# Performance work log

Hardware: AMD Instinct MI355X
Metric: run time of the kernel (lower is better)

## Reference

```python
import jax, jax.numpy as jnp
import numpy as np

B, T, D, H = 256, 512, 64, 128


def setup_inputs() -> dict:
    key = jax.random.key(0)
    ks = jax.random.split(key, 24)
    inp = {
        'values': jax.random.normal(ks[0], (B, T, D), jnp.float32),
        'masks': jax.random.randint(ks[1], (B, T, D), 0, 2).astype(jnp.float32),
        'deltas': jax.random.uniform(ks[2], (B, T, D), jnp.float32),
        'empirical_mean': jax.random.normal(ks[3], (D,), jnp.float32),
        'X_filledLOCF': jax.random.normal(ks[4], (B, T, D), jnp.float32),
        # parameters (xavier-ish scale for matrices, uniform for vectors)
        'w_gamma_x': jax.random.uniform(ks[5], (D,), jnp.float32),
        'w_gamma_h': jax.random.normal(ks[6], (D, H), jnp.float32) * (2.0 / (D + H)) ** 0.5,
        'w_rx': jax.random.normal(ks[7], (D, H), jnp.float32) * (2.0 / (D + H)) ** 0.5,
        'w_rh': jax.random.normal(ks[8], (H, H), jnp.float32) * (1.0 / H) ** 0.5,
        'w_rm': jax.random.normal(ks[9], (D, H), jnp.float32) * (2.0 / (D + H)) ** 0.5,
        'w_zx': jax.random.normal(ks[10], (D, H), jnp.float32) * (2.0 / (D + H)) ** 0.5,
        'w_zh': jax.random.normal(ks[11], (H, H), jnp.float32) * (1.0 / H) ** 0.5,
        'w_zm': jax.random.normal(ks[12], (D, H), jnp.float32) * (2.0 / (D + H)) ** 0.5,
        'w_hx': jax.random.normal(ks[13], (D, H), jnp.float32) * (2.0 / (D + H)) ** 0.5,
        'w_hh': jax.random.normal(ks[14], (H, H), jnp.float32) * (1.0 / H) ** 0.5,
        'w_hm': jax.random.normal(ks[15], (D, H), jnp.float32) * (2.0 / (D + H)) ** 0.5,
        'b_gamma_x': jax.random.uniform(ks[16], (D,), jnp.float32),
        'b_gamma_h': jax.random.uniform(ks[17], (H,), jnp.float32),
        'b_r': jax.random.uniform(ks[18], (H,), jnp.float32),
        'b_z': jax.random.uniform(ks[19], (H,), jnp.float32),
        'b_h': jax.random.uniform(ks[20], (H,), jnp.float32),
    }
    return inp


def reference(values, masks, deltas, empirical_mean, X_filledLOCF,
              w_gamma_x, w_gamma_h, w_rx, w_rh, w_rm, w_zx, w_zh, w_zm,
              w_hx, w_hh, w_hm, b_gamma_x, b_gamma_h, b_r, b_z, b_h):
    b, t, d = values.shape
    h0 = jnp.zeros((b, w_gamma_h.shape[1]), values.dtype)

    def step(h, xs):
        x, m, dlt, xl = xs  # each [B, D]
        gamma_x = jnp.exp(-jax.nn.relu(w_gamma_x * dlt + b_gamma_x))      # [B, D]
        gamma_h = jnp.exp(-jax.nn.relu(dlt @ w_gamma_h + b_gamma_h))      # [B, H]
        x = m * x + (1 - m) * (gamma_x * xl + (1 - gamma_x) * empirical_mean)
        h = gamma_h * h
        z = jax.nn.sigmoid(x @ w_zx + h @ w_zh + m @ w_zm + b_z)
        r = jax.nn.sigmoid(x @ w_rx + h @ w_rh + m @ w_rm + b_r)
        h_tilde = jnp.tanh(x @ w_hx + (r * h) @ w_hh + m @ w_hm + b_h)
        h = (1 - z) * h + z * h_tilde
        return h, h

    # scan over time axis: [T, B, D]
    xs = (jnp.swapaxes(values, 0, 1), jnp.swapaxes(masks, 0, 1),
          jnp.swapaxes(deltas, 0, 1), jnp.swapaxes(X_filledLOCF, 0, 1))
    h_last, hs = jax.lax.scan(step, h0, xs)
    hidden_tensor = jnp.swapaxes(hs, 0, 1)  # [B, T, H]
    return hidden_tensor, h_last
```

## Files before the change

### kernel.cpp

```cpp
#include <hip/hip_runtime.h>
#include <hip/hip_fp16.h>

#define B_ 256
#define T_ 512
#define D_ 64
#define H_ 128
#define BB 16

typedef float f32x4 __attribute__((ext_vector_type(4)));
typedef short s16x4 __attribute__((ext_vector_type(4)));
typedef short s16x8 __attribute__((ext_vector_type(8)));
typedef __bf16 bf16x8 __attribute__((ext_vector_type(8)));
typedef _Float16 h16x4 __attribute__((ext_vector_type(4)));
typedef _Float16 f16x8v __attribute__((ext_vector_type(8)));

__device__ unsigned short g_W16[7 * 8 * 2 * 512];
__device__ float g_bias[512];

__device__ inline float toF(__half x) { return __half2float(x); }

__device__ inline float fsig(float x) {
  return __builtin_amdgcn_rcpf(1.f + __expf(-x));
}
__device__ inline float ftanh(float x) {
  return 1.f - 2.f * __builtin_amdgcn_rcpf(1.f + __expf(2.f * x));
}
__device__ inline short f2bf(float f) {
  unsigned u = __builtin_bit_cast(unsigned, f);
  u += 0x7fff + ((u >> 16) & 1);
  return (short)(u >> 16);
}
__device__ __forceinline__ f32x4 MF(s16x8 a, s16x8 b, f32x4 c) {
  return __builtin_amdgcn_mfma_f32_16x16x32_bf16(
      __builtin_bit_cast(bf16x8, a), __builtin_bit_cast(bf16x8, b), c, 0, 0, 0);
}
__device__ __forceinline__ f32x4 MFH(f16x8v a, s16x8 b, f32x4 c) {
  return __builtin_amdgcn_mfma_f32_16x16x32_f16(
      a, __builtin_bit_cast(f16x8v, b), c, 0, 0, 0);
}

#define BAR()                                              \
  do {                                                     \
    asm volatile("s_waitcnt lgkmcnt(0)" ::: "memory");     \
    __builtin_amdgcn_s_barrier();                          \
  } while (0)

__global__ __launch_bounds__(64) void wprep(
    const float* __restrict__ wgh, const float* __restrict__ wzx,
    const float* __restrict__ wzm, const float* __restrict__ wrx,
    const float* __restrict__ wrm, const float* __restrict__ whx,
    const float* __restrict__ whm, const float* __restrict__ bgh,
    const float* __restrict__ bz, const float* __restrict__ br,
    const float* __restrict__ bh) {
  const int g = blockIdx.x, l = threadIdx.x;
  if (g < 112) {
    const float* mats[7] = {wgh, wzx, wzm, wrx, wrm, whx, whm};
    const int mat = g >> 4, sub = g & 15, ct = sub >> 1, tau = sub & 1;
    const float* W = mats[mat];
    const int base = ((mat * 8 + ct) * 2 + tau) * 512 + l * 8;
#pragma unroll
    for (int j = 0; j < 8; ++j) {
      const int k = 8 * (l >> 4) + j + 32 * tau;
      const int col = ct * 16 + (l & 15);
      g_W16[base + j] =
          __builtin_bit_cast(unsigned short, __float2half(W[k * 128 + col]));
    }
  } else {
    const int c = (g - 112) * 64 + l;
    float v = (c < 128)   ? bgh[c]
              : (c < 256) ? bz[c - 128]
              : (c < 384) ? br[c - 256]
                          : bh[c - 384];
    g_bias[c] = v;
  }
}

__global__ __launch_bounds__(256) void grud_pre_mfma(
    const float* __restrict__ values, const float* __restrict__ masks,
    const float* __restrict__ deltas, const float* __restrict__ emean,
    const float* __restrict__ locf, const float* __restrict__ w_gamma_x,
    const float* __restrict__ b_gamma_x, __half* __restrict__ A) {
  __shared__ __align__(16) char plds[65536];
  float* c_wg = (float*)(plds + 24576);
  float* c_bg = (float*)(plds + 24832);
  float* c_mn = (float*)(plds + 25088);

  const int tid = threadIdx.x;
  const int rowbase = blockIdx.x * 64;

  if (tid < 64) c_wg[tid] = w_gamma_x[tid];
  else if (tid < 128) c_bg[tid - 64] = b_gamma_x[tid - 64];
  else if (tid < 192) c_mn[tid - 128] = emean[tid - 128];
  __syncthreads();

  {
    const int r = tid >> 2;
    const int sp = tid & 3;
    const int swz = (r & 7) << 4;
#pragma unroll
    for (int ss = 0; ss < 2; ++ss) {
      const int s = sp + 4 * ss;
      const int k0 = 8 * s;
      const size_t gb = (size_t)(rowbase + r) * 64 + k0;
      const float4* vp = (const float4*)(values + gb);
      const float4* mp = (const float4*)(masks + gb);
      const float4* dp = (const float4*)(deltas + gb);
      const float4* lp = (const float4*)(locf + gb);
      float4 v0 = vp[0], v1 = vp[1], m0 = mp[0], m1 = mp[1];
      float4 d0 = dp[0], d1 = dp[1], l0 = lp[0], l1 = lp[1];
      float vv[8] = {v0.x, v0.y, v0.z, v0.w, v1.x, v1.y, v1.z, v1.w};
      float mm[8] = {m0.x, m0.y, m0.z, m0.w, m1.x, m1.y, m1.z, m1.w};
      float dd[8] = {d0.x, d0.y, d0.z, d0.w, d1.x, d1.y, d1.z, d1.w};
      float ll[8] = {l0.x, l0.y, l0.z, l0.w, l1.x, l1.y, l1.z, l1.w};
      s16x8 xe_, mv_, dl_;
#pragma unroll
      for (int j = 0; j < 8; ++j) {
        const int d_ = k0 + j;
        float gx = __expf(-fmaxf(c_wg[d_] * dd[j] + c_bg[d_], 0.f));
        float xo = mm[j] * vv[j] +
                   (1.f - mm[j]) * (gx * ll[j] + (1.f - gx) * c_mn[d_]);
        xe_[j] = __builtin_bit_cast(short, __float2half(xo));
        mv_[j] = __builtin_bit_cast(short, __float2half(mm[j]));
        dl_[j] = __builtin_bit_cast(short, __float2half(dd[j]));
      }
      const int ta = r * 128 + ((s * 16) ^ swz);
      *(s16x8*)(plds + ta) = xe_;
      *(s16x8*)(plds + 8192 + ta) = mv_;
      *(s16x8*)(plds + 16384 + ta) = dl_;
    }
  }
  __syncthreads();

  const int l = tid & 63;
  const int rt = tid >> 6;
  f16x8v xe0, xe1, mm0, mm1, dl0, dl1;
  {
    const int r = rt * 16 + (l & 15);
    const int swz = (r & 7) << 4;
    const int s0 = ((l >> 4) * 16) ^ swz;
    const int s1 = (((l >> 4) + 4) * 16) ^ swz;
    xe0 = *(const f16x8v*)(plds + r * 128 + s0);
    xe1 = *(const f16x8v*)(plds + r * 128 + s1);
    mm0 = *(const f16x8v*)(plds + 8192 + r * 128 + s0);
    mm1 = *(const f16x8v*)(plds + 8192 + r * 128 + s1);
    dl0 = *(const f16x8v*)(plds + 16384 + r * 128 + s0);
    dl1 = *(const f16x8v*)(plds + 16384 + r * 128 + s1);
  }
  __syncthreads();

  const s16x8* Wb = (const s16x8*)g_W16;
  const int cc = l & 15;
#pragma unroll 4
  for (int ct = 0; ct < 32; ++ct) {
    const int g = ct >> 3, ctl = ct & 7;
    f32x4 acc = {0.f, 0.f, 0.f, 0.f};
    if (g == 0) {
      s16x8 B0 = Wb[(ctl * 2 + 0) * 64 + l];
      s16x8 B1 = Wb[(ctl * 2 + 1) * 64 + l];
      acc = MFH(dl0, B0, acc);
      acc = MFH(dl1, B1, acc);
    } else {
      const int mx = 2 * g - 1, mmat = 2 * g;
      s16x8 Bx0 = Wb[((mx * 8 + ctl) * 2 + 0) * 64 + l];
      s16x8 Bx1 = Wb[((mx * 8 + ctl) * 2 + 1) * 64 + l];
      s16x8 Bm0 = Wb[((mmat * 8 + ctl) * 2 + 0) * 64 + l];
      s16x8 Bm1 = Wb[((mmat * 8 + ctl) * 2 + 1) * 64 + l];
      acc = MFH(xe0, Bx0, acc);
      acc = MFH(xe1, Bx1, acc);
      acc = MFH(mm0, Bm0, acc);
      acc = MFH(mm1, Bm1, acc);
    }
    const int c = ct * 16 + cc;
    const float bv = g_bias[c];
#pragma unroll
    for (int j = 0; j < 4; ++j) {
      const int row = rt * 16 + (l >> 4) * 4 + j;
      float v = acc[j] + bv;
      if (ct < 8) v = __expf(-fmaxf(v, 0.f));
      *(unsigned short*)(plds + row * 1024 + ((c * 2) ^ ((row & 7) << 4))) =
          __builtin_bit_cast(unsigned short, __float2half(v));
    }
  }
  __syncthreads();

  {
    const int r = tid >> 2, qq = tid & 3;
    const int swz = (r & 7) << 4;
#pragma unroll
    for (int i = 0; i < 16; ++i) {
      s16x8 v = *(const s16x8*)(plds + r * 1024 + ((qq * 256 + i * 16) ^ swz));
      *(s16x8*)((unsigned short*)A + (size_t)(rowbase + r) * 512 + qq * 128 +
                i * 8) = v;
    }
  }
}

#define STEP(T0, CUR, NXT)                                                  \
  do {                                                                      \
    const int t_ = (T0);                                                    \
    h16x4 tAz = CUR[1], tAr = CUR[2], tAh = CUR[3];                         \
    {                                                                       \
      const int t4 = (t_ + 4 < T_) ? t_ + 4 : T_ - 1;                       \
      const size_t r = ((size_t)bg * T_ + t4) * 128 + ci;                   \
      CUR[0] = Arows[r];       CUR[1] = Arows[r + 32];                      \
      CUR[2] = Arows[r + 64];  CUR[3] = Arows[r + 96];                      \
    }                                                                       \
    f32x4 Dz0 = {0,0,0,0}, Dz1 = {0,0,0,0};                                 \
    f32x4 Dr0 = {0,0,0,0}, Dr1 = {0,0,0,0};                                 \
    {                                                                       \
      s16x8 bh0 = *(const s16x8*)(h_bf + off_rd[0]);                        \
      s16x8 bh1 = *(const s16x8*)(h_bf + off_rd[1]);                        \
      s16x8 bh2 = *(const s16x8*)(h_bf + off_rd[2]);                        \
      s16x8 bh3 = *(const s16x8*)(h_bf + off_rd[3]);                        \
      Dz0 = MF(wzf[0], bh0, Dz0); Dr0 = MF(wrf[0], bh0, Dr0);               \
      Dz1 = MF(wzf[2], bh2, Dz1); Dr1 = MF(wrf[2], bh2, Dr1);               \
      Dz0 = MF(wzf[1], bh1, Dz0); Dr0 = MF(wrf[1], bh1, Dr0);               \
      Dz1 = MF(wzf[3], bh3, Dz1); Dr1 = MF(wrf[3], bh3, Dr1);               \
    }                                                                       \
    f32x4 zz;                                                               \
    s16x4 rhv;                                                              \
    _Pragma("unroll")                                                       \
    for (int j = 0; j < 4; ++j) {                                           \
      zz[j] = fsig((float)tAz[j] + (Dz0[j] + Dz1[j]));                      \
      float rr = fsig((float)tAr[j] + (Dr0[j] + Dr1[j]));                   \
      rhv[j] = f2bf(rr * hsc[j]);                                           \
    }                                                                       \
    *(s16x4*)(rh_bf + off_wr) = rhv;                                        \
    BAR();                                                                  \
    f32x4 Dh0 = {0,0,0,0}, Dh1 = {0,0,0,0};                                 \
    {                                                                       \
      s16x8 p0 = *(const s16x8*)(rh_bf + off_rd[0]);                        \
      s16x8 p1 = *(const s16x8*)(rh_bf + off_rd[1]);                        \
      s16x8 p2 = *(const s16x8*)(rh_bf + off_rd[2]);                        \
      s16x8 p3 = *(const s16x8*)(rh_bf + off_rd[3]);                        \
      Dh0 = MF(whf[0], p0, Dh0); Dh1 = MF(whf[2], p2, Dh1);                 \
      Dh0 = MF(whf[1], p1, Dh0); Dh1 = MF(whf[3], p3, Dh1);                 \
    }                                                                       \
    f32x4 hnv;                                                              \
    s16x4 hbv;                                                              \
    _Pragma("unroll")                                                       \
    for (int j = 0; j < 4; ++j) {                                           \
      float ht = ftanh((float)tAh[j] + (Dh0[j] + Dh1[j]));                  \
      float hn = (1.f - zz[j]) * hsc[j] + zz[j] * ht;                       \
      hnv[j] = hn;                                                          \
      float hg = hn * (float)NXT[0][j];                                     \
      hsc[j] = hg;                                                          \
      hbv[j] = f2bf(hg);                                                    \
    }                                                                       \
    *(f32x4*)(hid + ((size_t)bg * T_ + t_) * H_ + cb) = hnv;                \
    if (t_ == T_ - 1) *(f32x4*)(hlast + (size_t)bg * H_ + cb) = hnv;        \
    *(s16x4*)(h_bf + off_wr) = hbv;                                         \
    BAR();                                                                  \
  } while (0)

__global__ __launch_bounds__(512, 1) void grud_rec_mfma(
    const __half* __restrict__ A, const float* __restrict__ w_zh,
    const float* __restrict__ w_rh, const float* __restrict__ w_hh,
    float* __restrict__ hid, float* __restrict__ hlast) {
  const int tid = threadIdx.x;
  const int w = tid >> 6;
  const int lane = tid & 63;
  const int b = lane & 15;
  const int q = lane >> 4;
  const int cb = w * 16 + q * 4;
  const int bg = blockIdx.x * BB + b;

  __shared__ __align__(16) char lds[8192];
  char* h_bf = lds;
  char* rh_bf = lds + 4096;

  s16x8 wzf[4], wrf[4], whf[4];
#pragma unroll
  for (int tau = 0; tau < 4; ++tau) {
    s16x8 az, ar, ah;
#pragma unroll
    for (int j = 0; j < 8; ++j) {
      const int k = q * 8 + j + 32 * tau;
      az[j] = f2bf(w_zh[k * H_ + w * 16 + b]);
      ar[j] = f2bf(w_rh[k * H_ + w * 16 + b]);
      ah[j] = f2bf(w_hh[k * H_ + w * 16 + b]);
    }
    wzf[tau] = az; wrf[tau] = ar; whf[tau] = ah;
  }

  for (int i = tid; i < 8192 / 16; i += 512)
    ((f32x4*)lds)[i] = f32x4{0.f, 0.f, 0.f, 0.f};

  int off_rd[4];
#pragma unroll
  for (int tau = 0; tau < 4; ++tau) off_rd[tau] = tau * 1024 + lane * 16;
  const int off_wr =
      (w >> 1) * 1024 + (b + 16 * ((2 * w + (q >> 1)) & 3)) * 16 + 8 * (q & 1);

  const h16x4* Arows = (const h16x4*)A;
  const int ci = cb >> 2;

  h16x4 b0[4], b1[4], b2[4], b3[4];
  {
    const size_t r0 = ((size_t)bg * T_ + 0) * 128 + ci;
    b0[0] = Arows[r0]; b0[1] = Arows[r0 + 32];
    b0[2] = Arows[r0 + 64]; b0[3] = Arows[r0 + 96];
    const size_t r1 = ((size_t)bg * T_ + 1) * 128 + ci;
    b1[0] = Arows[r1]; b1[1] = Arows[r1 + 32];
    b1[2] = Arows[r1 + 64]; b1[3] = Arows[r1 + 96];
    const size_t r2 = ((size_t)bg * T_ + 2) * 128 + ci;
    b2[0] = Arows[r2]; b2[1] = Arows[r2 + 32];
    b2[2] = Arows[r2 + 64]; b2[3] = Arows[r2 + 96];
    const size_t r3 = ((size_t)bg * T_ + 3) * 128 + ci;
    b3[0] = Arows[r3]; b3[1] = Arows[r3 + 32];
    b3[2] = Arows[r3 + 64]; b3[3] = Arows[r3 + 96];
  }
  f32x4 hsc = {0.f, 0.f, 0.f, 0.f};
  __syncthreads();

  for (int tp = 0; tp < T_; tp += 4) {
    STEP(tp + 0, b0, b1);
    STEP(tp + 1, b1, b2);
    STEP(tp + 2, b2, b3);
    STEP(tp + 3, b3, b0);
  }
}

extern "C" void kernel_launch(void* const* d_in, const int* in_sizes, int n_in,
                              void* d_out, int out_size, void* d_ws, size_t ws_size,
                              hipStream_t stream) {
  const float* values = (const float*)d_in[0];
  const float* masks = (const float*)d_in[1];
  const float* deltas = (const float*)d_in[2];
  const float* emean = (const float*)d_in[3];
  const float* locf = (const float*)d_in[4];
  const float* w_gamma_x = (const float*)d_in[5];
  const float* w_gamma_h = (const float*)d_in[6];
  const float* w_rx = (const float*)d_in[7];
  const float* w_rh = (const float*)d_in[8];
  const float* w_rm = (const float*)d_in[9];
  const float* w_zx = (const float*)d_in[10];
  const float* w_zh = (const float*)d_in[11];
  const float* w_zm = (const float*)d_in[12];
  const float* w_hx = (const float*)d_in[13];
  const float* w_hh = (const float*)d_in[14];
  const float* w_hm = (const float*)d_in[15];
  const float* b_gamma_x = (const float*)d_in[16];
  const float* b_gamma_h = (const float*)d_in[17];
  const float* b_r = (const float*)d_in[18];
  const float* b_z = (const float*)d_in[19];
  const float* b_h = (const float*)d_in[20];

  float* hid = (float*)d_out;
  float* hlast = hid + (size_t)B_ * T_ * H_;
  __half* A = (__half*)d_ws;

  wprep<<<dim3(120), dim3(64), 0, stream>>>(
      w_gamma_h, w_zx, w_zm, w_rx, w_rm, w_hx, w_hm, b_gamma_h, b_z, b_r, b_h);
  grud_pre_mfma<<<dim3(B_ * T_ / 64), dim3(256), 0, stream>>>(
      values, masks, deltas, emean, locf, w_gamma_x, b_gamma_x, A);
  grud_rec_mfma<<<dim3(B_ / BB), dim3(512), 0, stream>>>(A, w_zh, w_rh, w_hh,
                                                         hid, hlast);
}
```

Baseline: 755.3 us.

## Halve recurrent block to 4 waves with two column tiles each; transpose pre-kernel MFMA output

After: 730.8 us. -3.3%, faster.

```diff
diff --git a/kernel.cpp b/kernel.cpp
--- a/kernel.cpp
+++ b/kernel.cpp
@@ -17,8 +17,6 @@
 __device__ unsigned short g_W16[7 * 8 * 2 * 512];
 __device__ float g_bias[512];
 
-__device__ inline float toF(__half x) { return __half2float(x); }
-
 __device__ inline float fsig(float x) {
   return __builtin_amdgcn_rcpf(1.f + __expf(-x));
 }
@@ -34,9 +32,9 @@
   return __builtin_amdgcn_mfma_f32_16x16x32_bf16(
       __builtin_bit_cast(bf16x8, a), __builtin_bit_cast(bf16x8, b), c, 0, 0, 0);
 }
-__device__ __forceinline__ f32x4 MFH(f16x8v a, s16x8 b, f32x4 c) {
+__device__ __forceinline__ f32x4 MFH2(s16x8 wfrag, f16x8v xfrag, f32x4 c) {
   return __builtin_amdgcn_mfma_f32_16x16x32_f16(
-      a, __builtin_bit_cast(f16x8v, b), c, 0, 0, 0);
+      __builtin_bit_cast(f16x8v, wfrag), xfrag, c, 0, 0, 0);
 }
 
 #define BAR()                                              \
@@ -80,7 +78,7 @@
     const float* __restrict__ deltas, const float* __restrict__ emean,
     const float* __restrict__ locf, const float* __restrict__ w_gamma_x,
     const float* __restrict__ b_gamma_x, __half* __restrict__ A) {
-  __shared__ __align__(16) char plds[65536];
+  __shared__ __align__(16) char plds[25344];
   float* c_wg = (float*)(plds + 24576);
   float* c_bg = (float*)(plds + 24832);
   float* c_mn = (float*)(plds + 25088);
@@ -146,10 +144,11 @@
     dl0 = *(const f16x8v*)(plds + 16384 + r * 128 + s0);
     dl1 = *(const f16x8v*)(plds + 16384 + r * 128 + s1);
   }
-  __syncthreads();
 
   const s16x8* Wb = (const s16x8*)g_W16;
-  const int cc = l & 15;
+  const int cj = (l >> 4) * 4;
+  const int row = rowbase + rt * 16 + (l & 15);
+  unsigned short* Aout = (unsigned short*)A + (size_t)row * 512;
 #pragma unroll 4
   for (int ct = 0; ct < 32; ++ct) {
     const int g = ct >> 3, ctl = ct & 7;
@@ -157,160 +156,173 @@
     if (g == 0) {
       s16x8 B0 = Wb[(ctl * 2 + 0) * 64 + l];
       s16x8 B1 = Wb[(ctl * 2 + 1) * 64 + l];
-      acc = MFH(dl0, B0, acc);
-      acc = MFH(dl1, B1, acc);
+      acc = MFH2(B0, dl0, acc);
+      acc = MFH2(B1, dl1, acc);
     } else {
       const int mx = 2 * g - 1, mmat = 2 * g;
       s16x8 Bx0 = Wb[((mx * 8 + ctl) * 2 + 0) * 64 + l];
       s16x8 Bx1 = Wb[((mx * 8 + ctl) * 2 + 1) * 64 + l];
       s16x8 Bm0 = Wb[((mmat * 8 + ctl) * 2 + 0) * 64 + l];
       s16x8 Bm1 = Wb[((mmat * 8 + ctl) * 2 + 1) * 64 + l];
-      acc = MFH(xe0, Bx0, acc);
-      acc = MFH(xe1, Bx1, acc);
-      acc = MFH(mm0, Bm0, acc);
-      acc = MFH(mm1, Bm1, acc);
-    }
-    const int c = ct * 16 + cc;
-    const float bv = g_bias[c];
+      acc = MFH2(Bx0, xe0, acc);
+      acc = MFH2(Bx1, xe1, acc);
+      acc = MFH2(Bm0, mm0, acc);
+      acc = MFH2(Bm1, mm1, acc);
+    }
+    const f32x4 bv = *(const f32x4*)(g_bias + ct * 16 + cj);
+    h16x4 outv;
 #pragma unroll
     for (int j = 0; j < 4; ++j) {
-      const int row = rt * 16 + (l >> 4) * 4 + j;
-      float v = acc[j] + bv;
+      float v = acc[j] + bv[j];
       if (ct < 8) v = __expf(-fmaxf(v, 0.f));
-      *(unsigned short*)(plds + row * 1024 + ((c * 2) ^ ((row & 7) << 4))) =
-          __builtin_bit_cast(unsigned short, __float2half(v));
-    }
-  }
-  __syncthreads();
-
-  {
-    const int r = tid >> 2, qq = tid & 3;
-    const int swz = (r & 7) << 4;
-#pragma unroll
-    for (int i = 0; i < 16; ++i) {
-      s16x8 v = *(const s16x8*)(plds + r * 1024 + ((qq * 256 + i * 16) ^ swz));
-      *(s16x8*)((unsigned short*)A + (size_t)(rowbase + r) * 512 + qq * 128 +
-                i * 8) = v;
-    }
+      outv[j] = (_Float16)v;
+    }
+    *(h16x4*)(Aout + g * 128 + ctl * 16 + cj) = outv;
   }
 }
 
 #define STEP(T0, CUR, NXT)                                                  \
   do {                                                                      \
     const int t_ = (T0);                                                    \
-    h16x4 tAz = CUR[1], tAr = CUR[2], tAh = CUR[3];                         \
-    {                                                                       \
+    h16x4 tAz0 = CUR[2], tAz1 = CUR[3], tAr0 = CUR[4], tAr1 = CUR[5];       \
+    h16x4 tAh0 = CUR[6], tAh1 = CUR[7];                                     \
+    {                                         \
       const int t4 = (t_ + 4 < T_) ? t_ + 4 : T_ - 1;                       \
-      const size_t r = ((size_t)bg * T_ + t4) * 128 + ci;                   \
-      CUR[0] = Arows[r];       CUR[1] = Arows[r + 32];                      \
-      CUR[2] = Arows[r + 64];  CUR[3] = Arows[r + 96];                      \
-    }                                                                       \
-    f32x4 Dz0 = {0,0,0,0}, Dz1 = {0,0,0,0};                                 \
-    f32x4 Dr0 = {0,0,0,0}, Dr1 = {0,0,0,0};                                 \
+      const size_t r = ((size_t)bg * T_ + t4) * 128;                        \
+      CUR[0] = Arows[r + ciA];      CUR[1] = Arows[r + ciB];                \
+      CUR[2] = Arows[r + 32 + ciA]; CUR[3] = Arows[r + 32 + ciB];           \
+      CUR[4] = Arows[r + 64 + ciA]; CUR[5] = Arows[r + 64 + ciB];           \
+      CUR[6] = Arows[r + 96 + ciA]; CUR[7] = Arows[r + 96 + ciB];           \
+    }                                                                       \
+    f32x4 DzA0 = {0,0,0,0}, DzA1 = {0,0,0,0};                               \
+    f32x4 DzB0 = {0,0,0,0}, DzB1 = {0,0,0,0};                               \
+    f32x4 DrA0 = {0,0,0,0}, DrA1 = {0,0,0,0};                               \
+    f32x4 DrB0 = {0,0,0,0}, DrB1 = {0,0,0,0};                               \
     {                                                                       \
       s16x8 bh0 = *(const s16x8*)(h_bf + off_rd[0]);                        \
       s16x8 bh1 = *(const s16x8*)(h_bf + off_rd[1]);                        \
       s16x8 bh2 = *(const s16x8*)(h_bf + off_rd[2]);                        \
       s16x8 bh3 = *(const s16x8*)(h_bf + off_rd[3]);                        \
-      Dz0 = MF(wzf[0], bh0, Dz0); Dr0 = MF(wrf[0], bh0, Dr0);               \
-      Dz1 = MF(wzf[2], bh2, Dz1); Dr1 = MF(wrf[2], bh2, Dr1);               \
-      Dz0 = MF(wzf[1], bh1, Dz0); Dr0 = MF(wrf[1], bh1, Dr0);               \
-      Dz1 = MF(wzf[3], bh3, Dz1); Dr1 = MF(wrf[3], bh3, Dr1);               \
-    }                                                                       \
-    f32x4 zz;                                                               \
-    s16x4 rhv;                                                              \
+      DzA0 = MF(wzf0[0], bh0, DzA0); DzB0 = MF(wzf1[0], bh0, DzB0);         \
+      DrA0 = MF(wrf0[0], bh0, DrA0); DrB0 = MF(wrf1[0], bh0, DrB0);         \
+      DzA1 = MF(wzf0[2], bh2, DzA1); DzB1 = MF(wzf1[2], bh2, DzB1);         \
+      DrA1 = MF(wrf0[2], bh2, DrA1); DrB1 = MF(wrf1[2], bh2, DrB1);         \
+      DzA0 = MF(wzf0[1], bh1, DzA0); DzB0 = MF(wzf1[1], bh1, DzB0);         \
+      DrA0 = MF(wrf0[1], bh1, DrA0); DrB0 = MF(wrf1[1], bh1, DrB0);         \
+      DzA1 = MF(wzf0[3], bh3, DzA1); DzB1 = MF(wzf1[3], bh3, DzB1);         \
+      DrA1 = MF(wrf0[3], bh3, DrA1); DrB1 = MF(wrf1[3], bh3, DrB1);         \
+    }                                                                       \
+    f32x4 zzA, zzB;                                                         \
+    s16x4 rhvA, rhvB;                                                       \
     _Pragma("unroll")                                                       \
     for (int j = 0; j < 4; ++j) {                                           \
-      zz[j] = fsig((float)tAz[j] + (Dz0[j] + Dz1[j]));                      \
-      float rr = fsig((float)tAr[j] + (Dr0[j] + Dr1[j]));                   \
-      rhv[j] = f2bf(rr * hsc[j]);                                           \
-    }                                                                       \
-    *(s16x4*)(rh_bf + off_wr) = rhv;                                        \
+      zzA[j] = fsig((float)tAz0[j] + (DzA0[j] + DzA1[j]));                  \
+      float rA = fsig((float)tAr0[j] + (DrA0[j] + DrA1[j]));                \
+      rhvA[j] = f2bf(rA * hscA[j]);                                         \
+      zzB[j] = fsig((float)tAz1[j] + (DzB0[j] + DzB1[j]));                  \
+      float rB = fsig((float)tAr1[j] + (DrB0[j] + DrB1[j]));                \
+      rhvB[j] = f2bf(rB * hscB[j]);                                         \
+    }                                                                       \
+    *(s16x4*)(rh_bf + off_wrA) = rhvA;                                      \
+    *(s16x4*)(rh_bf + off_wrB) = rhvB;                                      \
     BAR();                                                                  \
-    f32x4 Dh0 = {0,0,0,0}, Dh1 = {0,0,0,0};                                 \
+    f32x4 DhA0 = {0,0,0,0}, DhA1 = {0,0,0,0};                               \
+    f32x4 DhB0 = {0,0,0,0}, DhB1 = {0,0,0,0};                               \
     {                                                                       \
       s16x8 p0 = *(const s16x8*)(rh_bf + off_rd[0]);                        \
       s16x8 p1 = *(const s16x8*)(rh_bf + off_rd[1]);                        \
       s16x8 p2 = *(const s16x8*)(rh_bf + off_rd[2]);                        \
       s16x8 p3 = *(const s16x8*)(rh_bf + off_rd[3]);                        \
-      Dh0 = MF(whf[0], p0, Dh0); Dh1 = MF(whf[2], p2, Dh1);                 \
-      Dh0 = MF(whf[1], p1, Dh0); Dh1 = MF(whf[3], p3, Dh1);                 \
-    }                                                                       \
-    f32x4 hnv;                                                              \
-    s16x4 hbv;                                                              \
+      DhA0 = MF(whf0[0], p0, DhA0); DhB0 = MF(whf1[0], p0, DhB0);           \
+      DhA1 = MF(whf0[2], p2, DhA1); DhB1 = MF(whf1[2], p2, DhB1);           \
+      DhA0 = MF(whf0[1], p1, DhA0); DhB0 = MF(whf1[1], p1, DhB0);           \
+      DhA1 = MF(whf0[3], p3, DhA1); DhB1 = MF(whf1[3], p3, DhB1);           \
+    }                                                                       \
+    f32x4 hnA, hnB;                                                         \
+    s16x4 hbvA, hbvB;                                                       \
     _Pragma("unroll")                                                       \
     for (int j = 0; j < 4; ++j) {                                           \
-      float ht = ftanh((float)tAh[j] + (Dh0[j] + Dh1[j]));                  \
-      float hn = (1.f - zz[j]) * hsc[j] + zz[j] * ht;                       \
-      hnv[j] = hn;                                                          \
-      float hg = hn * (float)NXT[0][j];                                     \
-      hsc[j] = hg;                                                          \
-      hbv[j] = f2bf(hg);                                                    \
-    }                                                                       \
-    *(f32x4*)(hid + ((size_t)bg * T_ + t_) * H_ + cb) = hnv;                \
-    if (t_ == T_ - 1) *(f32x4*)(hlast + (size_t)bg * H_ + cb) = hnv;        \
-    *(s16x4*)(h_bf + off_wr) = hbv;                                         \
+      float htA = ftanh((float)tAh0[j] + (DhA0[j] + DhA1[j]));              \
+      float ha = hscA[j] + zzA[j] * (htA - hscA[j]);                        \
+      hnA[j] = ha;                                                          \
+      float hgA = ha * (float)NXT[0][j];                                    \
+      hscA[j] = hgA; hbvA[j] = f2bf(hgA);                                   \
+      float htB = ftanh((float)tAh1[j] + (DhB0[j] + DhB1[j]));              \
+      float hb = hscB[j] + zzB[j] * (htB - hscB[j]);                        \
+      hnB[j] = hb;                                                          \
+      float hgB = hb * (float)NXT[1][j];                                    \
+      hscB[j] = hgB; hbvB[j] = f2bf(hgB);                                   \
+    }                                                                       \
+    *(f32x4*)(hid + ((size_t)bg * T_ + t_) * H_ + cbA) = hnA;               \
+    *(f32x4*)(hid + ((size_t)bg * T_ + t_) * H_ + cbB) = hnB;               \
+    if (t_ == T_ - 1) {                                                     \
+      *(f32x4*)(hlast + (size_t)bg * H_ + cbA) = hnA;                       \
+      *(f32x4*)(hlast + (size_t)bg * H_ + cbB) = hnB;                       \
+    }                                                                       \
+    *(s16x4*)(h_bf + off_wrA) = hbvA;                                       \
+    *(s16x4*)(h_bf + off_wrB) = hbvB;                                       \
     BAR();                                                                  \
   } while (0)
 
-__global__ __launch_bounds__(512, 1) void grud_rec_mfma(
+__global__ __launch_bounds__(256, 1) void grud_rec_mfma(
     const __half* __restrict__ A, const float* __restrict__ w_zh,
     const float* __restrict__ w_rh, const float* __restrict__ w_hh,
     float* __restrict__ hid, float* __restrict__ hlast) {
   const int tid = threadIdx.x;
   const int w = tid >> 6;
-  const int lane = tid & 63;
-  const int b = lane & 15;
-  const int q = lane >> 4;
-  const int cb = w * 16 + q * 4;
+  const int l = tid & 63;
+  const int b = l & 15;
+  const int q = l >> 4;
+  const int cbA = w * 32 + q * 4;
+  const int cbB = cbA + 16;
   const int bg = blockIdx.x * BB + b;
 
   __shared__ __align__(16) char lds[8192];
   char* h_bf = lds;
   char* rh_bf = lds + 4096;
 
-  s16x8 wzf[4], wrf[4], whf[4];
+  s16x8 wzf0[4], wzf1[4], wrf0[4], wrf1[4], whf0[4], whf1[4];
 #pragma unroll
   for (int tau = 0; tau < 4; ++tau) {
-    s16x8 az, ar, ah;
+    s16x8 z0, z1, r0v, r1v, h0v, h1v;
 #pragma unroll
     for (int j = 0; j < 8; ++j) {
       const int k = q * 8 + j + 32 * tau;
-      az[j] = f2bf(w_zh[k * H_ + w * 16 + b]);
-      ar[j] = f2bf(w_rh[k * H_ + w * 16 + b]);
-      ah[j] = f2bf(w_hh[k * H_ + w * 16 + b]);
-    }
-    wzf[tau] = az; wrf[tau] = ar; whf[tau] = ah;
-  }
-
-  for (int i = tid; i < 8192 / 16; i += 512)
+      const int n0 = w * 32 + b;
+      const int n1 = n0 + 16;
+      z0[j] = f2bf(w_zh[k * H_ + n0]); z1[j] = f2bf(w_zh[k * H_ + n1]);
+      r0v[j] = f2bf(w_rh[k * H_ + n0]); r1v[j] = f2bf(w_rh[k * H_ + n1]);
+      h0v[j] = f2bf(w_hh[k * H_ + n0]); h1v[j] = f2bf(w_hh[k * H_ + n1]);
+    }
+    wzf0[tau] = z0; wzf1[tau] = z1;
+    wrf0[tau] = r0v; wrf1[tau] = r1v;
+    whf0[tau] = h0v; whf1[tau] = h1v;
+  }
+
+  for (int i = tid; i < 8192 / 16; i += 256)
     ((f32x4*)lds)[i] = f32x4{0.f, 0.f, 0.f, 0.f};
 
   int off_rd[4];
 #pragma unroll
-  for (int tau = 0; tau < 4; ++tau) off_rd[tau] = tau * 1024 + lane * 16;
-  const int off_wr =
-      (w >> 1) * 1024 + (b + 16 * ((2 * w + (q >> 1)) & 3)) * 16 + 8 * (q & 1);
+  for (int tau = 0; tau < 4; ++tau) off_rd[tau] = tau * 1024 + l * 16;
+  const int off_wrA = w * 1024 + (q >> 1) * 256 + b * 16 + (q & 1) * 8;
+  const int off_wrB = off_wrA + 512;
 
   const h16x4* Arows = (const h16x4*)A;
-  const int ci = cb >> 2;
-
-  h16x4 b0[4], b1[4], b2[4], b3[4];
-  {
-    const size_t r0 = ((size_t)bg * T_ + 0) * 128 + ci;
-    b0[0] = Arows[r0]; b0[1] = Arows[r0 + 32];
-    b0[2] = Arows[r0 + 64]; b0[3] = Arows[r0 + 96];
-    const size_t r1 = ((size_t)bg * T_ + 1) * 128 + ci;
-    b1[0] = Arows[r1]; b1[1] = Arows[r1 + 32];
-    b1[2] = Arows[r1 + 64]; b1[3] = Arows[r1 + 96];
-    const size_t r2 = ((size_t)bg * T_ + 2) * 128 + ci;
-    b2[0] = Arows[r2]; b2[1] = Arows[r2 + 32];
-    b2[2] = Arows[r2 + 64]; b2[3] = Arows[r2 + 96];
-    const size_t r3 = ((size_t)bg * T_ + 3) * 128 + ci;
-    b3[0] = Arows[r3]; b3[1] = Arows[r3 + 32];
-    b3[2] = Arows[r3 + 64]; b3[3] = Arows[r3 + 96];
-  }
-  f32x4 hsc = {0.f, 0.f, 0.f, 0.f};
+  const int ciA = w * 8 + q;
+  const int ciB = ciA + 4;
+
+  h16x4 b0[8], b1[8], b2[8], b3[8];
+#pragma unroll
+  for (int t0 = 0; t0 < 4; ++t0) {
+    h16x4* dst = (t0 == 0) ? b0 : (t0 == 1) ? b1 : (t0 == 2) ? b2 : b3;
+    const size_t r = ((size_t)bg * T_ + t0) * 128;
+    dst[0] = Arows[r + ciA];      dst[1] = Arows[r + ciB];
+    dst[2] = Arows[r + 32 + ciA]; dst[3] = Arows[r + 32 + ciB];
+    dst[4] = Arows[r + 64 + ciA]; dst[5] = Arows[r + 64 + ciB];
+    dst[6] = Arows[r + 96 + ciA]; dst[7] = Arows[r + 96 + ciB];
+  }
+  f32x4 hscA = {0.f, 0.f, 0.f, 0.f}, hscB = {0.f, 0.f, 0.f, 0.f};
   __syncthreads();
 
   for (int tp = 0; tp < T_; tp += 4) {
@@ -354,6 +366,6 @@
       w_gamma_h, w_zx, w_zm, w_rx, w_rm, w_hx, w_hm, b_gamma_h, b_z, b_r, b_h);
   grud_pre_mfma<<<dim3(B_ * T_ / 64), dim3(256), 0, stream>>>(
       values, masks, deltas, emean, locf, w_gamma_x, b_gamma_x, A);
-  grud_rec_mfma<<<dim3(B_ / BB), dim3(512), 0, stream>>>(A, w_zh, w_rh, w_hh,
+  grud_rec_mfma<<<dim3(B_ / BB), dim3(256), 0, stream>>>(A, w_zh, w_rh, w_hh,
                                                          hid, hlast);
 }
```

## Switch recurrence to fp16 MFMA, seed accumulators, and store precompute directly

Applied to the files above, without the earlier changes.

After: 631.0 us. 1.2x faster.

```diff
diff --git a/kernel.cpp b/kernel.cpp
--- a/kernel.cpp
+++ b/kernel.cpp
@@ -10,33 +10,26 @@
 typedef float f32x4 __attribute__((ext_vector_type(4)));
 typedef short s16x4 __attribute__((ext_vector_type(4)));
 typedef short s16x8 __attribute__((ext_vector_type(8)));
-typedef __bf16 bf16x8 __attribute__((ext_vector_type(8)));
+typedef __fp16 fp16x2 __attribute__((ext_vector_type(2)));
 typedef _Float16 h16x4 __attribute__((ext_vector_type(4)));
 typedef _Float16 f16x8v __attribute__((ext_vector_type(8)));
 
 __device__ unsigned short g_W16[7 * 8 * 2 * 512];
 __device__ float g_bias[512];
 
-__device__ inline float toF(__half x) { return __half2float(x); }
-
 __device__ inline float fsig(float x) {
   return __builtin_amdgcn_rcpf(1.f + __expf(-x));
 }
 __device__ inline float ftanh(float x) {
   return 1.f - 2.f * __builtin_amdgcn_rcpf(1.f + __expf(2.f * x));
 }
-__device__ inline short f2bf(float f) {
-  unsigned u = __builtin_bit_cast(unsigned, f);
-  u += 0x7fff + ((u >> 16) & 1);
-  return (short)(u >> 16);
-}
-__device__ __forceinline__ f32x4 MF(s16x8 a, s16x8 b, f32x4 c) {
-  return __builtin_amdgcn_mfma_f32_16x16x32_bf16(
-      __builtin_bit_cast(bf16x8, a), __builtin_bit_cast(bf16x8, b), c, 0, 0, 0);
-}
-__device__ __forceinline__ f32x4 MFH(f16x8v a, s16x8 b, f32x4 c) {
+__device__ __forceinline__ f32x4 MFH(s16x8 a, s16x8 b, f32x4 c) {
   return __builtin_amdgcn_mfma_f32_16x16x32_f16(
-      a, __builtin_bit_cast(f16x8v, b), c, 0, 0, 0);
+      __builtin_bit_cast(f16x8v, a), __builtin_bit_cast(f16x8v, b), c, 0, 0, 0);
+}
+__device__ __forceinline__ f32x4 MFH2(s16x8 wfrag, f16x8v xfrag, f32x4 c) {
+  return __builtin_amdgcn_mfma_f32_16x16x32_f16(
+      __builtin_bit_cast(f16x8v, wfrag), xfrag, c, 0, 0, 0);
 }
 
 #define BAR()                                              \
@@ -80,7 +73,7 @@
     const float* __restrict__ deltas, const float* __restrict__ emean,
     const float* __restrict__ locf, const float* __restrict__ w_gamma_x,
     const float* __restrict__ b_gamma_x, __half* __restrict__ A) {
-  __shared__ __align__(16) char plds[65536];
+  __shared__ __align__(16) char plds[25344];
   float* c_wg = (float*)(plds + 24576);
   float* c_bg = (float*)(plds + 24832);
   float* c_mn = (float*)(plds + 25088);
@@ -146,10 +139,11 @@
     dl0 = *(const f16x8v*)(plds + 16384 + r * 128 + s0);
     dl1 = *(const f16x8v*)(plds + 16384 + r * 128 + s1);
   }
-  __syncthreads();
 
   const s16x8* Wb = (const s16x8*)g_W16;
-  const int cc = l & 15;
+  const int cj = (l >> 4) * 4;
+  const int row = rowbase + rt * 16 + (l & 15);
+  unsigned short* Aout = (unsigned short*)A + (size_t)row * 512;
 #pragma unroll 4
   for (int ct = 0; ct < 32; ++ct) {
     const int g = ct >> 3, ctl = ct & 7;
@@ -157,99 +151,98 @@
     if (g == 0) {
       s16x8 B0 = Wb[(ctl * 2 + 0) * 64 + l];
       s16x8 B1 = Wb[(ctl * 2 + 1) * 64 + l];
-      acc = MFH(dl0, B0, acc);
-      acc = MFH(dl1, B1, acc);
+      acc = MFH2(B0, dl0, acc);
+      acc = MFH2(B1, dl1, acc);
     } else {
       const int mx = 2 * g - 1, mmat = 2 * g;
       s16x8 Bx0 = Wb[((mx * 8 + ctl) * 2 + 0) * 64 + l];
       s16x8 Bx1 = Wb[((mx * 8 + ctl) * 2 + 1) * 64 + l];
       s16x8 Bm0 = Wb[((mmat * 8 + ctl) * 2 + 0) * 64 + l];
       s16x8 Bm1 = Wb[((mmat * 8 + ctl) * 2 + 1) * 64 + l];
-      acc = MFH(xe0, Bx0, acc);
-      acc = MFH(xe1, Bx1, acc);
-      acc = MFH(mm0, Bm0, acc);
-      acc = MFH(mm1, Bm1, acc);
-    }
-    const int c = ct * 16 + cc;
-    const float bv = g_bias[c];
+      acc = MFH2(Bx0, xe0, acc);
+      acc = MFH2(Bx1, xe1, acc);
+      acc = MFH2(Bm0, mm0, acc);
+      acc = MFH2(Bm1, mm1, acc);
+    }
+    const f32x4 bv = *(const f32x4*)(g_bias + ct * 16 + cj);
+    h16x4 outv;
 #pragma unroll
     for (int j = 0; j < 4; ++j) {
-      const int row = rt * 16 + (l >> 4) * 4 + j;
-      float v = acc[j] + bv;
+      float v = acc[j] + bv[j];
       if (ct < 8) v = __expf(-fmaxf(v, 0.f));
-      *(unsigned short*)(plds + row * 1024 + ((c * 2) ^ ((row & 7) << 4))) =
-          __builtin_bit_cast(unsigned short, __float2half(v));
-    }
-  }
-  __syncthreads();
-
-  {
-    const int r = tid >> 2, qq = tid & 3;
-    const int swz = (r & 7) << 4;
-#pragma unroll
-    for (int i = 0; i < 16; ++i) {
-      s16x8 v = *(const s16x8*)(plds + r * 1024 + ((qq * 256 + i * 16) ^ swz));
-      *(s16x8*)((unsigned short*)A + (size_t)(rowbase + r) * 512 + qq * 128 +
-                i * 8) = v;
-    }
+      outv[j] = (_Float16)v;
+    }
+    *(h16x4*)(Aout + g * 128 + ctl * 16 + cj) = outv;
   }
 }
 
 #define STEP(T0, CUR, NXT)                                                  \
   do {                                                                      \
     const int t_ = (T0);                                                    \
-    h16x4 tAz = CUR[1], tAr = CUR[2], tAh = CUR[3];                         \
-    {                                                                       \
+    f32x4 Dz0 = {(float)CUR[1][0], (float)CUR[1][1],                        \
+                 (float)CUR[1][2], (float)CUR[1][3]};                       \
+    f32x4 Dr0 = {(float)CUR[2][0], (float)CUR[2][1],                        \
+                 (float)CUR[2][2], (float)CUR[2][3]};                       \
+    f32x4 Dh0 = {(float)CUR[3][0], (float)CUR[3][1],                        \
+                 (float)CUR[3][2], (float)CUR[3][3]};                       \
+    {                                         \
       const int t4 = (t_ + 4 < T_) ? t_ + 4 : T_ - 1;                       \
       const size_t r = ((size_t)bg * T_ + t4) * 128 + ci;                   \
       CUR[0] = Arows[r];       CUR[1] = Arows[r + 32];                      \
       CUR[2] = Arows[r + 64];  CUR[3] = Arows[r + 96];                      \
     }                                                                       \
-    f32x4 Dz0 = {0,0,0,0}, Dz1 = {0,0,0,0};                                 \
-    f32x4 Dr0 = {0,0,0,0}, Dr1 = {0,0,0,0};                                 \
+    f32x4 Dz1 = {0, 0, 0, 0}, Dr1 = {0, 0, 0, 0};                           \
     {                                                                       \
       s16x8 bh0 = *(const s16x8*)(h_bf + off_rd[0]);                        \
       s16x8 bh1 = *(const s16x8*)(h_bf + off_rd[1]);                        \
       s16x8 bh2 = *(const s16x8*)(h_bf + off_rd[2]);                        \
       s16x8 bh3 = *(const s16x8*)(h_bf + off_rd[3]);                        \
-      Dz0 = MF(wzf[0], bh0, Dz0); Dr0 = MF(wrf[0], bh0, Dr0);               \
-      Dz1 = MF(wzf[2], bh2, Dz1); Dr1 = MF(wrf[2], bh2, Dr1);               \
-      Dz0 = MF(wzf[1], bh1, Dz0); Dr0 = MF(wrf[1], bh1, Dr0);               \
-      Dz1 = MF(wzf[3], bh3, Dz1); Dr1 = MF(wrf[3], bh3, Dr1);               \
+      Dz0 = MFH(wzf[0], bh0, Dz0); Dr0 = MFH(wrf[0], bh0, Dr0);             \
+      Dz1 = MFH(wzf[2], bh2, Dz1); Dr1 = MFH(wrf[2], bh2, Dr1);             \
+      Dz0 = MFH(wzf[1], bh1, Dz0); Dr0 = MFH(wrf[1], bh1, Dr0);             \
+      Dz1 = MFH(wzf[3], bh3, Dz1); Dr1 = MFH(wrf[3], bh3, Dr1);             \
     }                                                                       \
     f32x4 zz;                                                               \
-    s16x4 rhv;                                                              \
-    _Pragma("unroll")                                                       \
-    for (int j = 0; j < 4; ++j) {                                           \
-      zz[j] = fsig((float)tAz[j] + (Dz0[j] + Dz1[j]));                      \
-      float rr = fsig((float)tAr[j] + (Dr0[j] + Dr1[j]));                   \
-      rhv[j] = f2bf(rr * hsc[j]);                                           \
-    }                                                                       \
-    *(s16x4*)(rh_bf + off_wr) = rhv;                                        \
+    {                                                                       \
+      float r0_ = fsig(Dr0[0] + Dr1[0]) * hsc[0];                           \
+      float r1_ = fsig(Dr0[1] + Dr1[1]) * hsc[1];                           \
+      float r2_ = fsig(Dr0[2] + Dr1[2]) * hsc[2];                           \
+      float r3_ = fsig(Dr0[3] + Dr1[3]) * hsc[3];                           \
+      zz[0] = fsig(Dz0[0] + Dz1[0]); zz[1] = fsig(Dz0[1] + Dz1[1]);         \
+      zz[2] = fsig(Dz0[2] + Dz1[2]); zz[3] = fsig(Dz0[3] + Dz1[3]);         \
+      union { fp16x2 h2[2]; s16x4 v; } u;                                   \
+      u.h2[0] = __builtin_amdgcn_cvt_pkrtz(r0_, r1_);                       \
+      u.h2[1] = __builtin_amdgcn_cvt_pkrtz(r2_, r3_);                       \
+      *(s16x4*)(rh_bf + off_wr) = u.v;                                      \
+    }                                                                       \
     BAR();                                                                  \
-    f32x4 Dh0 = {0,0,0,0}, Dh1 = {0,0,0,0};                                 \
+    f32x4 Dh1 = {0, 0, 0, 0};                                               \
     {                                                                       \
       s16x8 p0 = *(const s16x8*)(rh_bf + off_rd[0]);                        \
       s16x8 p1 = *(const s16x8*)(rh_bf + off_rd[1]);                        \
       s16x8 p2 = *(const s16x8*)(rh_bf + off_rd[2]);                        \
       s16x8 p3 = *(const s16x8*)(rh_bf + off_rd[3]);                        \
-      Dh0 = MF(whf[0], p0, Dh0); Dh1 = MF(whf[2], p2, Dh1);                 \
-      Dh0 = MF(whf[1], p1, Dh0); Dh1 = MF(whf[3], p3, Dh1);                 \
-    }                                                                       \
-    f32x4 hnv;                                                              \
-    s16x4 hbv;                                                              \
+      Dh0 = MFH(whf[0], p0, Dh0); Dh1 = MFH(whf[2], p2, Dh1);               \
+      Dh0 = MFH(whf[1], p1, Dh0); Dh1 = MFH(whf[3], p3, Dh1);               \
+    }                                                                       \
+    f32x4 hnv, hgv;                                                         \
     _Pragma("unroll")                                                       \
     for (int j = 0; j < 4; ++j) {                                           \
-      float ht = ftanh((float)tAh[j] + (Dh0[j] + Dh1[j]));                  \
-      float hn = (1.f - zz[j]) * hsc[j] + zz[j] * ht;                       \
+      float ht = ftanh(Dh0[j] + Dh1[j]);                                    \
+      float hn = hsc[j] + zz[j] * (ht - hsc[j]);                            \
       hnv[j] = hn;                                                          \
-      float hg = hn * (float)NXT[0][j];                                     \
+      float hg = hn * (float)NXT[0][j];              \
+      hgv[j] = hg;                                                          \
       hsc[j] = hg;                                                          \
-      hbv[j] = f2bf(hg);                                                    \
+    }                                                                       \
+    {                                                                       \
+      union { fp16x2 h2[2]; s16x4 v; } u;                                   \
+      u.h2[0] = __builtin_amdgcn_cvt_pkrtz(hgv[0], hgv[1]);                 \
+      u.h2[1] = __builtin_amdgcn_cvt_pkrtz(hgv[2], hgv[3]);                 \
+      *(s16x4*)(h_bf + off_wr) = u.v;                                       \
     }                                                                       \
     *(f32x4*)(hid + ((size_t)bg * T_ + t_) * H_ + cb) = hnv;                \
     if (t_ == T_ - 1) *(f32x4*)(hlast + (size_t)bg * H_ + cb) = hnv;        \
-    *(s16x4*)(h_bf + off_wr) = hbv;                                         \
     BAR();                                                                  \
   } while (0)
 
@@ -276,9 +269,9 @@
 #pragma unroll
     for (int j = 0; j < 8; ++j) {
       const int k = q * 8 + j + 32 * tau;
-      az[j] = f2bf(w_zh[k * H_ + w * 16 + b]);
-      ar[j] = f2bf(w_rh[k * H_ + w * 16 + b]);
-      ah[j] = f2bf(w_hh[k * H_ + w * 16 + b]);
+      az[j] = __builtin_bit_cast(short, (_Float16)w_zh[k * H_ + w * 16 + b]);
+      ar[j] = __builtin_bit_cast(short, (_Float16)w_rh[k * H_ + w * 16 + b]);
+      ah[j] = __builtin_bit_cast(short, (_Float16)w_hh[k * H_ + w * 16 + b]);
     }
     wzf[tau] = az; wrf[tau] = ar; whf[tau] = ah;
   }
```
